# Kernel optimization log

Measured on AMD Instinct MI355X. Metric: run time of the kernel, lower is better.

The kernel has to match this reference:

```python
import jax, jax.numpy as jnp
import numpy as np

HIDDEN = 1024
FFN = 4096
NUM_EXPERTS = 8
TOP_K = 2
BATCH, SEQ = 2, 2048


def setup_inputs() -> dict:
    key = jax.random.key(0)
    ks = jax.random.split(key, 6)
    s_h = 1.0 / np.sqrt(HIDDEN)
    s_f = 1.0 / np.sqrt(FFN)
    return {
        "hidden_states": jax.random.normal(ks[0], (BATCH, SEQ, HIDDEN), jnp.float32),
        "gate_w": jax.random.uniform(ks[1], (HIDDEN, NUM_EXPERTS), jnp.float32, -s_h, s_h),
        "gate_b": jax.random.uniform(ks[2], (NUM_EXPERTS,), jnp.float32, -s_h, s_h),
        "w1": jax.random.uniform(ks[3], (NUM_EXPERTS, HIDDEN, FFN), jnp.float32, -s_h, s_h),
        "w3": jax.random.uniform(ks[4], (NUM_EXPERTS, HIDDEN, FFN), jnp.float32, -s_h, s_h),
        "w2": jax.random.uniform(ks[5], (NUM_EXPERTS, FFN, HIDDEN), jnp.float32, -s_f, s_f),
    }


def reference(hidden_states, gate_w, gate_b, w1, w3, w2):
    B, S, D = hidden_states.shape
    T = B * S
    x = hidden_states.reshape(T, D)

    # Router: softmax in fp32, top-2, renormalize (matches torch source)
    logits = x @ gate_w + gate_b                       # [T, E]
    probs = jax.nn.softmax(logits.astype(jnp.float32), axis=-1)
    top_w, top_idx = jax.lax.top_k(probs, TOP_K)       # [T, 2]
    top_w = top_w / jnp.sum(top_w, axis=-1, keepdims=True)

    # Dense combine weights [T, E]: zero for unselected experts.
    combine = jnp.zeros((T, NUM_EXPERTS), jnp.float32)
    combine = combine.at[jnp.arange(T)[:, None], top_idx].set(top_w)
    combine = combine.astype(x.dtype)

    # Grouped SwiGLU expert MLPs (vectorized over experts, zero-weight tokens
    # contribute nothing after combine).
    h = jax.nn.silu(jnp.einsum('td,edf->tef', x, w1)) * jnp.einsum('td,edf->tef', x, w3)
    out_e = jnp.einsum('tef,efd->ted', h, w2)          # [T, E, D]
    out = jnp.einsum('ted,te->td', out_e, combine)     # weighted combine
    return out.reshape(B, S, D)
```

## Files before the change

### kernel.cpp

```cpp
#include <hip/hip_runtime.h>


#define NTOK 4096
#define HID  1024
#define FFN  4096
#define NE   8
#define TM   128
#define CAP  9216
#define MAXT 72

typedef __bf16 bf16x8 __attribute__((ext_vector_type(8)));
typedef float  f32x4  __attribute__((ext_vector_type(4)));

typedef __attribute__((address_space(3))) unsigned int       lds_uint;
typedef const __attribute__((address_space(1))) unsigned int glob_uint;

__device__ __forceinline__ unsigned short f2bf(float f) {
  union { float f; unsigned u; } v; v.f = f;
  return (unsigned short)((v.u + 0x7FFFu + ((v.u >> 16) & 1u)) >> 16);
}

__device__ __forceinline__ void gload16(const void* g, void* l) {
  __builtin_amdgcn_global_load_lds((glob_uint*)g, (lds_uint*)l, 16, 0, 0);
}

__global__ void k0_zero_cvt(const float* __restrict__ x,
                            unsigned short* __restrict__ xbf,
                            float* __restrict__ out,
                            int* __restrict__ counts) {
  int i = blockIdx.x * 256 + threadIdx.x;
  const float4* x4 = (const float4*)x;
  float4 v = x4[i];
  uint2 p;
  p.x = (unsigned)f2bf(v.x) | ((unsigned)f2bf(v.y) << 16);
  p.y = (unsigned)f2bf(v.z) | ((unsigned)f2bf(v.w) << 16);
  ((uint2*)xbf)[i] = p;
  ((float4*)out)[i] = make_float4(0.f, 0.f, 0.f, 0.f);
  if (i < NE) counts[i] = 0;
}

__global__ void k1_transpose(const float* __restrict__ src,
                             unsigned short* __restrict__ dst,
                             int Rfull, int Cfull, int r0, int c0,
                             int RW, int CW) {
  __shared__ unsigned short tile[32][33];
  size_t mb = blockIdx.z;
  src += mb * (size_t)Rfull * Cfull;
  dst += mb * (size_t)RW * CW;
  int j  = blockIdx.x * 32 + threadIdx.x;
  int i0 = blockIdx.y * 32;
#pragma unroll
  for (int u = 0; u < 4; u++) {
    int i = i0 + threadIdx.y + u * 8;
    tile[threadIdx.y + u * 8][threadIdx.x] = f2bf(src[(size_t)(r0 + i) * Cfull + c0 + j]);
  }
  __syncthreads();
  int i = i0 + threadIdx.x;
#pragma unroll
  for (int u = 0; u < 4; u++) {
    int jj = blockIdx.x * 32 + threadIdx.y + u * 8;
    dst[(size_t)jj * RW + i] = tile[threadIdx.x][threadIdx.y + u * 8];
  }
}

__global__ void k2_router(const float* __restrict__ x,
                          const float* __restrict__ gw,
                          const float* __restrict__ gb,
                          int* __restrict__ topi, float* __restrict__ topw,
                          int* __restrict__ counts) {
  int wid = threadIdx.x >> 6, lane = threadIdx.x & 63;
  int t = blockIdx.x * 4 + wid;
  const float4* x4 = (const float4*)(x + (size_t)t * HID);
  const float4* g4 = (const float4*)gw;
  float acc[8];
#pragma unroll
  for (int e = 0; e < 8; e++) acc[e] = 0.f;
#pragma unroll
  for (int i = 0; i < 4; i++) {
    float4 xv = x4[i * 64 + lane];
    int dbase = (i * 64 + lane) * 4;
    float xs[4] = {xv.x, xv.y, xv.z, xv.w};
#pragma unroll
    for (int j = 0; j < 4; j++) {
      float4 ga  = g4[(dbase + j) * 2];
      float4 gbv = g4[(dbase + j) * 2 + 1];
      acc[0] += xs[j] * ga.x;  acc[1] += xs[j] * ga.y;
      acc[2] += xs[j] * ga.z;  acc[3] += xs[j] * ga.w;
      acc[4] += xs[j] * gbv.x; acc[5] += xs[j] * gbv.y;
      acc[6] += xs[j] * gbv.z; acc[7] += xs[j] * gbv.w;
    }
  }
#pragma unroll
  for (int e = 0; e < 8; e++)
#pragma unroll
    for (int m = 1; m < 64; m <<= 1) acc[e] += __shfl_xor(acc[e], m);
  if (lane == 0) {
    float lg[8];
#pragma unroll
    for (int e = 0; e < 8; e++) lg[e] = acc[e] + gb[e];
    int i0 = 0; float m0 = lg[0];
#pragma unroll
    for (int e = 1; e < 8; e++) if (lg[e] > m0) { m0 = lg[e]; i0 = e; }
    int i1 = -1; float m1 = -1e30f;
#pragma unroll
    for (int e = 0; e < 8; e++) if (e != i0 && lg[e] > m1) { m1 = lg[e]; i1 = e; }
    float w0 = 1.f / (1.f + __expf(m1 - m0));
    topi[2 * t] = i0; topi[2 * t + 1] = i1;
    topw[2 * t] = w0; topw[2 * t + 1] = 1.f - w0;
    atomicAdd(&counts[i0], 1);
    atomicAdd(&counts[i1], 1);
  }
}

__global__ void k3_scan(const int* __restrict__ counts, int* offs, int* fill,
                        int* tile_e, int* tile_row,
                        int* sorted_tok, float* sorted_w) {
  if (threadIdx.x == 0) {
    int off = 0, tt = 0;
    for (int e = 0; e < NE; e++) {
      offs[e] = off; fill[e] = 0;
      int nt = (counts[e] + TM - 1) >> 7;
      for (int j = 0; j < nt; j++) { tile_e[tt] = e; tile_row[tt] = off + j * TM; tt++; }
      off += nt * TM;
    }
    for (; tt < MAXT; tt++) { tile_e[tt] = -1; tile_row[tt] = 0; }
  }
  for (int i = threadIdx.x; i < CAP; i += 256) { sorted_tok[i] = 0; sorted_w[i] = 0.f; }
}

__global__ void k4_scatter(const int* __restrict__ topi, const float* __restrict__ topw,
                           const int* __restrict__ offs, int* __restrict__ fill,
                           int* __restrict__ sorted_tok, float* __restrict__ sorted_w) {
  int t = blockIdx.x * 256 + threadIdx.x;
#pragma unroll
  for (int k = 0; k < 2; k++) {
    int e = topi[2 * t + k];
    int p = atomicAdd(&fill[e], 1);
    int s = offs[e] + p;
    sorted_tok[s] = t;
    sorted_w[s]   = topw[2 * t + k];
  }
}

__global__ __launch_bounds__(256) void k5_gemm_h(
    const unsigned short* __restrict__ xbf,
    const unsigned short* __restrict__ w1t,
    const unsigned short* __restrict__ w3t,
    unsigned short* __restrict__ h,
    const int* __restrict__ tile_e, const int* __restrict__ tile_row,
    const int* __restrict__ sorted_tok, int FC) {
  __shared__ unsigned short lsA[128 * 32];
  __shared__ unsigned short lsB1[64 * 32];
  __shared__ unsigned short lsB3[64 * 32];

  int tile = blockIdx.x;
  int e = tile_e[tile];
  if (e < 0) return;
  int row0 = tile_row[tile];
  int n0 = blockIdx.y * 64;
  int tid = threadIdx.x;

  int kc = tid & 3, lr = tid >> 2;
  int tok0 = sorted_tok[row0 + lr];
  int tok1 = sorted_tok[row0 + lr + 64];
  const unsigned short* ga0 = xbf + (size_t)tok0 * HID + kc * 8;
  const unsigned short* ga1 = xbf + (size_t)tok1 * HID + kc * 8;
  const unsigned short* gb1 = w1t + ((size_t)e * FC + n0 + lr) * HID + kc * 8;
  const unsigned short* gb3 = w3t + ((size_t)e * FC + n0 + lr) * HID + kc * 8;
  unsigned short* la0 = lsA  + tid * 8;
  unsigned short* la1 = lsA  + (256 + tid) * 8;
  unsigned short* lb1 = lsB1 + tid * 8;
  unsigned short* lb3 = lsB3 + tid * 8;

  int wid = tid >> 6, lane = tid & 63, lm = lane & 15, q = lane >> 4;
  int wr = wid >> 1, wc = wid & 1;
  const unsigned short* As  = lsA  + (wr * 64 + lm) * 32 + q * 8;
  const unsigned short* B1s = lsB1 + (wc * 32 + lm) * 32 + q * 8;
  const unsigned short* B3s = lsB3 + (wc * 32 + lm) * 32 + q * 8;

  f32x4 acc1[4][2] = {};
  f32x4 acc3[4][2] = {};

#pragma unroll 1
  for (int ks = 0; ks < HID / 32; ks++) {
    __syncthreads();
    int k0 = ks * 32;
    gload16(ga0 + k0, la0);
    gload16(ga1 + k0, la1);
    gload16(gb1 + k0, lb1);
    gload16(gb3 + k0, lb3);
    __syncthreads();
    bf16x8 a[4], b1f[2], b3f[2];
#pragma unroll
    for (int ti = 0; ti < 4; ti++) a[ti] = *(const bf16x8*)(As + ti * 512);
#pragma unroll
    for (int tj = 0; tj < 2; tj++) {
      b1f[tj] = *(const bf16x8*)(B1s + tj * 512);
      b3f[tj] = *(const bf16x8*)(B3s + tj * 512);
    }
#pragma unroll
    for (int ti = 0; ti < 4; ti++)
#pragma unroll
      for (int tj = 0; tj < 2; tj++) {
        acc1[ti][tj] = __builtin_amdgcn_mfma_f32_16x16x32_bf16(a[ti], b1f[tj], acc1[ti][tj], 0, 0, 0);
        acc3[ti][tj] = __builtin_amdgcn_mfma_f32_16x16x32_bf16(a[ti], b3f[tj], acc3[ti][tj], 0, 0, 0);
      }
  }

#pragma unroll
  for (int ti = 0; ti < 4; ti++)
#pragma unroll
    for (int tj = 0; tj < 2; tj++)
#pragma unroll
      for (int r = 0; r < 4; r++) {
        float v1 = acc1[ti][tj][r];
        float v3 = acc3[ti][tj][r];
        float hv = (v1 / (1.f + __expf(-v1))) * v3;
        int grow = row0 + wr * 64 + ti * 16 + q * 4 + r;
        int gcol = n0 + wc * 32 + tj * 16 + lm;
        h[(size_t)grow * FC + gcol] = f2bf(hv);
      }
}

__global__ __launch_bounds__(256) void k6_gemm_out(
    const unsigned short* __restrict__ h,
    const unsigned short* __restrict__ w2t,
    float* __restrict__ out,
    const int* __restrict__ tile_e, const int* __restrict__ tile_row,
    const int* __restrict__ sorted_tok, const float* __restrict__ sorted_w,
    int FC) {
  __shared__ unsigned short lsA[128 * 32];
  __shared__ unsigned short lsB[128 * 32];
  __shared__ int   toks[128];
  __shared__ float wts[128];

  int tile = blockIdx.x;
  int e = tile_e[tile];
  if (e < 0) return;
  int row0 = tile_row[tile];
  int n0 = blockIdx.y * 128;
  int tid = threadIdx.x;

  if (tid < 128) { toks[tid] = sorted_tok[row0 + tid]; wts[tid] = sorted_w[row0 + tid]; }

  int kc = tid & 3, lr = tid >> 2;
  const unsigned short* ga0 = h + (size_t)(row0 + lr) * FC + kc * 8;
  const unsigned short* ga1 = h + (size_t)(row0 + lr + 64) * FC + kc * 8;
  const unsigned short* gb0 = w2t + ((size_t)e * HID + n0 + lr) * FC + kc * 8;
  const unsigned short* gb1 = w2t + ((size_t)e * HID + n0 + lr + 64) * FC + kc * 8;
  unsigned short* la0 = lsA + tid * 8;
  unsigned short* la1 = lsA + (256 + tid) * 8;
  unsigned short* lb0 = lsB + tid * 8;
  unsigned short* lb1 = lsB + (256 + tid) * 8;

  int wid = tid >> 6, lane = tid & 63, lm = lane & 15, q = lane >> 4;
  int wr = wid >> 1, wc = wid & 1;
  const unsigned short* As = lsA + (wr * 64 + lm) * 32 + q * 8;
  const unsigned short* Bs = lsB + (wc * 64 + lm) * 32 + q * 8;

  f32x4 acc[4][4] = {};

#pragma unroll 1
  for (int ks = 0; ks < FC / 32; ks++) {
    __syncthreads();
    int k0 = ks * 32;
    gload16(ga0 + k0, la0);
    gload16(ga1 + k0, la1);
    gload16(gb0 + k0, lb0);
    gload16(gb1 + k0, lb1);
    __syncthreads();
    bf16x8 a[4], b[4];
#pragma unroll
    for (int ti = 0; ti < 4; ti++) a[ti] = *(const bf16x8*)(As + ti * 512);
#pragma unroll
    for (int tj = 0; tj < 4; tj++) b[tj] = *(const bf16x8*)(Bs + tj * 512);
#pragma unroll
    for (int ti = 0; ti < 4; ti++)
#pragma unroll
      for (int tj = 0; tj < 4; tj++)
        acc[ti][tj] = __builtin_amdgcn_mfma_f32_16x16x32_bf16(a[ti], b[tj], acc[ti][tj], 0, 0, 0);
  }

#pragma unroll
  for (int ti = 0; ti < 4; ti++)
#pragma unroll
    for (int r = 0; r < 4; r++) {
      int lrow = wr * 64 + ti * 16 + q * 4 + r;
      float wt = wts[lrow];
      if (wt != 0.f) {
        int trow = toks[lrow];
#pragma unroll
        for (int tj = 0; tj < 4; tj++) {
          int gcol = n0 + wc * 64 + tj * 16 + lm;
          atomicAdd(&out[(size_t)trow * HID + gcol], acc[ti][tj][r] * wt);
        }
      }
    }
}

extern "C" void kernel_launch(void* const* d_in, const int* in_sizes, int n_in,
                              void* d_out, int out_size, void* d_ws, size_t ws_size,
                              hipStream_t stream) {
  const float* x  = (const float*)d_in[0];
  const float* gw = (const float*)d_in[1];
  const float* gb = (const float*)d_in[2];
  const float* w1 = (const float*)d_in[3];
  const float* w3 = (const float*)d_in[4];
  const float* w2 = (const float*)d_in[5];
  float* out = (float*)d_out;

  char* ws = (char*)d_ws;
  int*   counts     = (int*)(ws + 0);
  int*   fill       = counts + 8;
  int*   offs       = fill + 8;
  int*   tile_e     = offs + 8;
  int*   tile_row   = tile_e + 80;
  int*   topi       = (int*)(ws + 1024);
  float* topw       = (float*)(ws + 33792);
  int*   sorted_tok = (int*)(ws + 66560);
  float* sorted_w   = (float*)(ws + 103424);
  unsigned short* xbf = (unsigned short*)(ws + 147456);
  const size_t base = 8536064ull;

  int FC = FFN;
  while (FC > 64) {
    size_t W  = (size_t)NE * FC * HID * 2;
    size_t Hb = (size_t)CAP * FC * 2;
    if (base + 3 * W + Hb <= ws_size) break;
    FC >>= 1;
  }
  size_t W = (size_t)NE * FC * HID * 2;
  unsigned short* w1t  = (unsigned short*)(ws + base);
  unsigned short* w3t  = (unsigned short*)(ws + base + W);
  unsigned short* w2t  = (unsigned short*)(ws + base + 2 * W);
  unsigned short* hbuf = (unsigned short*)(ws + base + 3 * W);
  int nc = FFN / FC;

  k0_zero_cvt<<<4096, 256, 0, stream>>>(x, xbf, out, counts);
  k2_router<<<1024, 256, 0, stream>>>(x, gw, gb, topi, topw, counts);
  k3_scan<<<1, 256, 0, stream>>>(counts, offs, fill, tile_e, tile_row, sorted_tok, sorted_w);
  k4_scatter<<<16, 256, 0, stream>>>(topi, topw, offs, fill, sorted_tok, sorted_w);

  for (int c = 0; c < nc; c++) {
    int c0 = c * FC;
    k1_transpose<<<dim3(FC / 32, HID / 32, NE), dim3(32, 8), 0, stream>>>(
        w1, w1t, HID, FFN, 0, c0, HID, FC);
    k1_transpose<<<dim3(FC / 32, HID / 32, NE), dim3(32, 8), 0, stream>>>(
        w3, w3t, HID, FFN, 0, c0, HID, FC);
    k1_transpose<<<dim3(HID / 32, FC / 32, NE), dim3(32, 8), 0, stream>>>(
        w2, w2t, FFN, HID, c0, 0, FC, HID);
    k5_gemm_h<<<dim3(MAXT, FC / 64), 256, 0, stream>>>(
        xbf, w1t, w3t, hbuf, tile_e, tile_row, sorted_tok, FC);
    k6_gemm_out<<<dim3(MAXT, HID / 128), 256, 0, stream>>>(
        hbuf, w2t, out, tile_e, tile_row, sorted_tok, sorted_w, FC);
  }
}
```

Measured before the change: 948.9 us.

## Vectorize weight transpose, merge w1/w3 launches, swizzle LDS, template FC

The weight transpose now works on 64x64 tiles with float4 loads and 16-byte stores, and one launch covers both w1 and w3. Both expert GEMMs XOR-swizzle the 8-element k-chunk in shared memory (global source offsets and fragment read offsets use matching swizzles) to cut LDS bank conflicts. The GEMMs are templated on the FFN chunk size so strides and loop bounds become compile-time constants. The per-call fp32-to-bf16 weight transpose is memory-bound and likely a large share of time, so faster transposes plus conflict-free LDS reads target both phases.

```diff
diff --git a/kernel.cpp b/kernel.cpp
--- a/kernel.cpp
+++ b/kernel.cpp
@@ -39,27 +39,40 @@
   if (i < NE) counts[i] = 0;
 }
 
-__global__ void k1_transpose(const float* __restrict__ src,
-                             unsigned short* __restrict__ dst,
-                             int Rfull, int Cfull, int r0, int c0,
-                             int RW, int CW) {
-  __shared__ unsigned short tile[32][33];
-  size_t mb = blockIdx.z;
-  src += mb * (size_t)Rfull * Cfull;
-  dst += mb * (size_t)RW * CW;
-  int j  = blockIdx.x * 32 + threadIdx.x;
-  int i0 = blockIdx.y * 32;
+__global__ __launch_bounds__(256) void k1_transpose(
+    const float* __restrict__ s0, unsigned short* __restrict__ d0,
+    const float* __restrict__ s1, unsigned short* __restrict__ d1,
+    int Rfull, int Cfull, int rg0, int cg0, int RW, int CW) {
+  __shared__ unsigned short tile[64 * 72];
+  int z = blockIdx.z;
+  const float* src = (z < 8 ? s0 : s1) + (size_t)(z & 7) * Rfull * Cfull;
+  unsigned short* dst = (z < 8 ? d0 : d1) + (size_t)(z & 7) * RW * CW;
+  int c0 = blockIdx.x * 64;
+  int r0 = blockIdx.y * 64;
+  int t = threadIdx.x;
+  int q = t >> 4, p = t & 15;
+
+  const float4* s4 = (const float4*)(src + (size_t)(rg0 + r0 + 4 * q) * Cfull
+                                     + cg0 + c0) + p;
+  unsigned short v[4][4];
 #pragma unroll
   for (int u = 0; u < 4; u++) {
-    int i = i0 + threadIdx.y + u * 8;
-    tile[threadIdx.y + u * 8][threadIdx.x] = f2bf(src[(size_t)(r0 + i) * Cfull + c0 + j]);
+    float4 xv = s4[(size_t)u * (Cfull >> 2)];
+    v[u][0] = f2bf(xv.x); v[u][1] = f2bf(xv.y);
+    v[u][2] = f2bf(xv.z); v[u][3] = f2bf(xv.w);
+  }
+#pragma unroll
+  for (int j = 0; j < 4; j++) {
+    ushort4 w = make_ushort4(v[0][j], v[1][j], v[2][j], v[3][j]);
+    *(ushort4*)&tile[(4 * p + j) * 72 + 4 * q] = w;
   }
   __syncthreads();
-  int i = i0 + threadIdx.x;
-#pragma unroll
-  for (int u = 0; u < 4; u++) {
-    int jj = blockIdx.x * 32 + threadIdx.y + u * 8;
-    dst[(size_t)jj * RW + i] = tile[threadIdx.x][threadIdx.y + u * 8];
+  int b = t & 7;
+#pragma unroll
+  for (int vi = 0; vi < 2; vi++) {
+    int c = (t >> 3) + 32 * vi;
+    uint4 w = *(const uint4*)&tile[c * 72 + 8 * b];
+    *(uint4*)(dst + (size_t)(c0 + c) * RW + r0 + 8 * b) = w;
   }
 }
 
@@ -142,13 +155,16 @@
   }
 }
 
+
+template<int CFC>
 __global__ __launch_bounds__(256) void k5_gemm_h(
     const unsigned short* __restrict__ xbf,
     const unsigned short* __restrict__ w1t,
     const unsigned short* __restrict__ w3t,
     unsigned short* __restrict__ h,
     const int* __restrict__ tile_e, const int* __restrict__ tile_row,
-    const int* __restrict__ sorted_tok, int FC) {
+    const int* __restrict__ sorted_tok, int FCdyn) {
+  const int FC = CFC ? CFC : FCdyn;
   __shared__ unsigned short lsA[128 * 32];
   __shared__ unsigned short lsB1[64 * 32];
   __shared__ unsigned short lsB3[64 * 32];
@@ -161,12 +177,13 @@
   int tid = threadIdx.x;
 
   int kc = tid & 3, lr = tid >> 2;
+  int g = (kc ^ ((lr >> 1) & 3)) * 8;
   int tok0 = sorted_tok[row0 + lr];
   int tok1 = sorted_tok[row0 + lr + 64];
-  const unsigned short* ga0 = xbf + (size_t)tok0 * HID + kc * 8;
-  const unsigned short* ga1 = xbf + (size_t)tok1 * HID + kc * 8;
-  const unsigned short* gb1 = w1t + ((size_t)e * FC + n0 + lr) * HID + kc * 8;
-  const unsigned short* gb3 = w3t + ((size_t)e * FC + n0 + lr) * HID + kc * 8;
+  const unsigned short* ga0 = xbf + (size_t)tok0 * HID + g;
+  const unsigned short* ga1 = xbf + (size_t)tok1 * HID + g;
+  const unsigned short* gb1 = w1t + ((size_t)e * FC + n0 + lr) * HID + g;
+  const unsigned short* gb3 = w3t + ((size_t)e * FC + n0 + lr) * HID + g;
   unsigned short* la0 = lsA  + tid * 8;
   unsigned short* la1 = lsA  + (256 + tid) * 8;
   unsigned short* lb1 = lsB1 + tid * 8;
@@ -174,9 +191,10 @@
 
   int wid = tid >> 6, lane = tid & 63, lm = lane & 15, q = lane >> 4;
   int wr = wid >> 1, wc = wid & 1;
-  const unsigned short* As  = lsA  + (wr * 64 + lm) * 32 + q * 8;
-  const unsigned short* B1s = lsB1 + (wc * 32 + lm) * 32 + q * 8;
-  const unsigned short* B3s = lsB3 + (wc * 32 + lm) * 32 + q * 8;
+  int qs = (q ^ ((lm >> 1) & 3)) * 8;
+  const unsigned short* As  = lsA  + (wr * 64 + lm) * 32 + qs;
+  const unsigned short* B1s = lsB1 + (wc * 32 + lm) * 32 + qs;
+  const unsigned short* B3s = lsB3 + (wc * 32 + lm) * 32 + qs;
 
   f32x4 acc1[4][2] = {};
   f32x4 acc3[4][2] = {};
@@ -222,13 +240,15 @@
       }
 }
 
+template<int CFC>
 __global__ __launch_bounds__(256) void k6_gemm_out(
     const unsigned short* __restrict__ h,
     const unsigned short* __restrict__ w2t,
     float* __restrict__ out,
     const int* __restrict__ tile_e, const int* __restrict__ tile_row,
     const int* __restrict__ sorted_tok, const float* __restrict__ sorted_w,
-    int FC) {
+    int FCdyn) {
+  const int FC = CFC ? CFC : FCdyn;
   __shared__ unsigned short lsA[128 * 32];
   __shared__ unsigned short lsB[128 * 32];
   __shared__ int   toks[128];
@@ -244,10 +264,11 @@
   if (tid < 128) { toks[tid] = sorted_tok[row0 + tid]; wts[tid] = sorted_w[row0 + tid]; }
 
   int kc = tid & 3, lr = tid >> 2;
-  const unsigned short* ga0 = h + (size_t)(row0 + lr) * FC + kc * 8;
-  const unsigned short* ga1 = h + (size_t)(row0 + lr + 64) * FC + kc * 8;
-  const unsigned short* gb0 = w2t + ((size_t)e * HID + n0 + lr) * FC + kc * 8;
-  const unsigned short* gb1 = w2t + ((size_t)e * HID + n0 + lr + 64) * FC + kc * 8;
+  int g = (kc ^ ((lr >> 1) & 3)) * 8;
+  const unsigned short* ga0 = h + (size_t)(row0 + lr) * FC + g;
+  const unsigned short* ga1 = h + (size_t)(row0 + lr + 64) * FC + g;
+  const unsigned short* gb0 = w2t + ((size_t)e * HID + n0 + lr) * FC + g;
+  const unsigned short* gb1 = w2t + ((size_t)e * HID + n0 + lr + 64) * FC + g;
   unsigned short* la0 = lsA + tid * 8;
   unsigned short* la1 = lsA + (256 + tid) * 8;
   unsigned short* lb0 = lsB + tid * 8;
@@ -255,8 +276,9 @@
 
   int wid = tid >> 6, lane = tid & 63, lm = lane & 15, q = lane >> 4;
   int wr = wid >> 1, wc = wid & 1;
-  const unsigned short* As = lsA + (wr * 64 + lm) * 32 + q * 8;
-  const unsigned short* Bs = lsB + (wc * 64 + lm) * 32 + q * 8;
+  int qs = (q ^ ((lm >> 1) & 3)) * 8;
+  const unsigned short* As = lsA + (wr * 64 + lm) * 32 + qs;
+  const unsigned short* Bs = lsB + (wc * 64 + lm) * 32 + qs;
 
   f32x4 acc[4][4] = {};
 
@@ -343,15 +365,30 @@
 
   for (int c = 0; c < nc; c++) {
     int c0 = c * FC;
-    k1_transpose<<<dim3(FC / 32, HID / 32, NE), dim3(32, 8), 0, stream>>>(
-        w1, w1t, HID, FFN, 0, c0, HID, FC);
-    k1_transpose<<<dim3(FC / 32, HID / 32, NE), dim3(32, 8), 0, stream>>>(
-        w3, w3t, HID, FFN, 0, c0, HID, FC);
-    k1_transpose<<<dim3(HID / 32, FC / 32, NE), dim3(32, 8), 0, stream>>>(
-        w2, w2t, FFN, HID, c0, 0, FC, HID);
-    k5_gemm_h<<<dim3(MAXT, FC / 64), 256, 0, stream>>>(
-        xbf, w1t, w3t, hbuf, tile_e, tile_row, sorted_tok, FC);
-    k6_gemm_out<<<dim3(MAXT, HID / 128), 256, 0, stream>>>(
-        hbuf, w2t, out, tile_e, tile_row, sorted_tok, sorted_w, FC);
-  }
-}
+    k1_transpose<<<dim3(FC / 64, HID / 64, 16), 256, 0, stream>>>(
+        w1, w1t, w3, w3t, HID, FFN, 0, c0, HID, FC);
+    k1_transpose<<<dim3(HID / 64, FC / 64, 8), 256, 0, stream>>>(
+        w2, w2t, nullptr, nullptr, FFN, HID, c0, 0, FC, HID);
+    if (FC == 4096) {
+      k5_gemm_h<4096><<<dim3(MAXT, FC / 64), 256, 0, stream>>>(
+          xbf, w1t, w3t, hbuf, tile_e, tile_row, sorted_tok, FC);
+      k6_gemm_out<4096><<<dim3(MAXT, HID / 128), 256, 0, stream>>>(
+          hbuf, w2t, out, tile_e, tile_row, sorted_tok, sorted_w, FC);
+    } else if (FC == 2048) {
+      k5_gemm_h<2048><<<dim3(MAXT, FC / 64), 256, 0, stream>>>(
+          xbf, w1t, w3t, hbuf, tile_e, tile_row, sorted_tok, FC);
+      k6_gemm_out<2048><<<dim3(MAXT, HID / 128), 256, 0, stream>>>(
+          hbuf, w2t, out, tile_e, tile_row, sorted_tok, sorted_w, FC);
+    } else if (FC == 1024) {
+      k5_gemm_h<1024><<<dim3(MAXT, FC / 64), 256, 0, stream>>>(
+          xbf, w1t, w3t, hbuf, tile_e, tile_row, sorted_tok, FC);
+      k6_gemm_out<1024><<<dim3(MAXT, HID / 128), 256, 0, stream>>>(
+          hbuf, w2t, out, tile_e, tile_row, sorted_tok, sorted_w, FC);
+    } else {
+      k5_gemm_h<0><<<dim3(MAXT, FC / 64), 256, 0, stream>>>(
+          xbf, w1t, w3t, hbuf, tile_e, tile_row, sorted_tok, FC);
+      k6_gemm_out<0><<<dim3(MAXT, HID / 128), 256, 0, stream>>>(
+          hbuf, w2t, out, tile_e, tile_row, sorted_tok, sorted_w, FC);
+    }
+  }
+}
```

Measured after the change: 939.4 us. No clear change (-1.0%).
